# Optimization experiments

Hardware: AMD Instinct MI355X
Metric: run time of the kernel (lower is better)

The kernel has to match this reference:

```python
import jax, jax.numpy as jnp
import numpy as np

N_HEAD = 12


def setup_inputs() -> dict:
    key = jax.random.key(0)
    ks = jax.random.split(key, 5)
    B, T, C = 2, 2048, 768
    x = jax.random.normal(ks[0], (B, T, C), dtype=jnp.float32)
    w_attn = jax.random.normal(ks[1], (3 * C, C), dtype=jnp.float32) * 0.02
    b_attn = jax.random.normal(ks[2], (3 * C,), dtype=jnp.float32) * 0.02
    w_proj = jax.random.normal(ks[3], (C, C), dtype=jnp.float32) * 0.02
    b_proj = jax.random.normal(ks[4], (C,), dtype=jnp.float32) * 0.02
    return {"x": x, "w_attn": w_attn, "b_attn": b_attn, "w_proj": w_proj, "b_proj": b_proj}


def reference(x, w_attn, b_attn, w_proj, b_proj):
    B, T, C = x.shape
    H = N_HEAD
    D = C // H
    # fused QKV projection (torch Linear: x @ W.T + b)
    qkv = x @ w_attn.T + b_attn                      # [B, T, 3C]
    q, k, v = jnp.split(qkv, 3, axis=-1)
    q = q.reshape(B, T, H, D).transpose(0, 2, 1, 3)  # [B, H, T, D]
    k = k.reshape(B, T, H, D).transpose(0, 2, 1, 3)
    v = v.reshape(B, T, H, D).transpose(0, 2, 1, 3)
    # NOTE: original scales by 1/sqrt(k.size(0)) == 1/sqrt(B) (batch!), reproduced faithfully
    scale = 1.0 / jnp.sqrt(jnp.asarray(B, dtype=x.dtype))
    scores = jnp.einsum("bhtd,bhsd->bhts", q, k) * scale  # [B, H, T, T]
    causal = jnp.tril(jnp.ones((T, T), dtype=bool))
    scores = jnp.where(causal[None, None], scores, jnp.asarray(-jnp.inf, dtype=x.dtype))
    attn = jax.nn.softmax(scores, axis=-1)
    # dropout layers are identity in eval mode
    out = jnp.einsum("bhts,bhsd->bhtd", attn, v)     # [B, H, T, D]
    out = out.transpose(0, 2, 1, 3).reshape(B, T, C)
    return out @ w_proj.T + b_proj
```

## Files before the change

kernel.cpp:

```cpp
#include <hip/hip_runtime.h>
#include <hip/hip_bf16.h>
#include <stdint.h>

typedef __bf16 bf16;
typedef __bf16 bf16x4 __attribute__((ext_vector_type(4)));
typedef __bf16 bf16x8 __attribute__((ext_vector_type(8)));
typedef float f32x4 __attribute__((ext_vector_type(4)));

__device__ __forceinline__ f32x4 mfma16(bf16x8 a, bf16x8 b, f32x4 c) {
    return __builtin_amdgcn_mfma_f32_16x16x32_bf16(a, b, c, 0, 0, 0);
}

__device__ __forceinline__ void gload_lds16(const void* g, void* l) {
    __builtin_amdgcn_global_load_lds((__attribute__((address_space(1))) void*)g,
                                     (__attribute__((address_space(3))) void*)l,
                                     16, 0, 0);
}

__global__ void k_cast3(const float* __restrict__ x, const float* __restrict__ wa,
                        const float* __restrict__ wp, bf16* __restrict__ xb,
                        bf16* __restrict__ wab, bf16* __restrict__ wpb) {
    const int N1 = 786432, N2 = 442368, N3 = 147456;
    int i = blockIdx.x * blockDim.x + threadIdx.x;
    int stride = gridDim.x * blockDim.x;
    for (; i < N1 + N2 + N3; i += stride) {
        const float* src; bf16* dst; int j = i;
        if (j < N1)           { src = x;  dst = xb; }
        else if (j < N1 + N2) { src = wa; dst = wab; j -= N1; }
        else                  { src = wp; dst = wpb; j -= N1 + N2; }
        float4 v = reinterpret_cast<const float4*>(src)[j];
        bf16x4 o = { (bf16)v.x, (bf16)v.y, (bf16)v.z, (bf16)v.w };
        reinterpret_cast<bf16x4*>(dst)[j] = o;
    }
}

template<bool BF16_OUT>
__global__ __launch_bounds__(256) void k_gemm_bt(
        const bf16* __restrict__ A, const bf16* __restrict__ W,
        const float* __restrict__ bias, void* __restrict__ Cout,
        int M, int N, int K) {
    __shared__ bf16 As[128 * 32];
    __shared__ bf16 Ws[128 * 32];
    const int tid = threadIdx.x;
    const int l = tid & 63, w = tid >> 6;
    const int lr = l & 15, lq = l >> 4;
    const int wm = w >> 1, wn = w & 1;
    const int bm = blockIdx.y * 128, bn = blockIdx.x * 128;

    f32x4 acc[4][4] = {};

    for (int k0 = 0; k0 < K; k0 += 32) {
        __syncthreads();
        #pragma unroll
        for (int i = 0; i < 2; ++i) {
            int c = tid + i * 256;
            int row = c >> 2, c8 = (c & 3) * 8;
            gload_lds16(A + (size_t)(bm + row) * K + k0 + c8, As + c * 8);
            gload_lds16(W + (size_t)(bn + row) * K + k0 + c8, Ws + c * 8);
        }
        __syncthreads();
        bf16x8 af[4], wf[4];
        #pragma unroll
        for (int f = 0; f < 4; ++f) {
            af[f] = *reinterpret_cast<const bf16x8*>(As + (wm * 64 + f * 16 + lr) * 32 + lq * 8);
            wf[f] = *reinterpret_cast<const bf16x8*>(Ws + (wn * 64 + f * 16 + lr) * 32 + lq * 8);
        }
        #pragma unroll
        for (int fm = 0; fm < 4; ++fm)
            #pragma unroll
            for (int fn = 0; fn < 4; ++fn)
                acc[fm][fn] = mfma16(af[fm], wf[fn], acc[fm][fn]);
    }

    #pragma unroll
    for (int fm = 0; fm < 4; ++fm) {
        #pragma unroll
        for (int fn = 0; fn < 4; ++fn) {
            int row = bm + wm * 64 + fm * 16 + lq * 4;
            int col = bn + wn * 64 + fn * 16 + lr;
            float bv = bias[col];
            #pragma unroll
            for (int r = 0; r < 4; ++r) {
                float v = acc[fm][fn][r] + bv;
                if (BF16_OUT)
                    ((bf16*)Cout)[(size_t)(row + r) * N + col] = (bf16)v;
                else
                    ((float*)Cout)[(size_t)(row + r) * N + col] = v;
            }
        }
    }
}

#define CLOG2E 1.02014439f

__global__ __launch_bounds__(256, 3) void k_flash_attn(
        const bf16* __restrict__ qkv, bf16* __restrict__ att) {
    __shared__ bf16 Ks[3][4096];
    __shared__ bf16 Vt[2][64][72];

    const int tid = threadIdx.x;
    const int l = tid & 63, w = tid >> 6;
    const int lr = l & 15, lq = l >> 4;

    const int bid = blockIdx.x;
    const int s = bid >> 8, i = (bid >> 3) & 31, t7 = bid & 7;
    int qb;
    if (s == 0)      qb = i;
    else if (s == 2) qb = (i + 16) & 31;
    else             qb = (i < 8) ? (31 - 2 * i) : (i < 16) ? (30 - 2 * i)
                       : (i < 24) ? (62 - 2 * i) : (63 - 2 * i);
    const int hb = s * 8 + t7;
    const int h = hb % 12, b = hb / 12;

    const bf16* Qp = qkv + (size_t)b * 2048 * 2304 + h * 64;
    const bf16* Kp = Qp + 768;
    const bf16* Vp = Qp + 1536;

    const int qr0 = qb * 64 + w * 16;

    bf16x8 qf[2];
    #pragma unroll
    for (int ks = 0; ks < 2; ++ks)
        qf[ks] = *reinterpret_cast<const bf16x8*>(
            Qp + (size_t)(qr0 + lr) * 2304 + ks * 32 + lq * 8);

    f32x4 o[4] = {};
    float lsum = 0.f;

    auto stageK = [&](int buf, int kv0) {
        #pragma unroll
        for (int ii = 0; ii < 2; ++ii) {
            int c = tid + ii * 256;
            int row = c >> 3, j = c & 7;
            gload_lds16(Kp + (size_t)(kv0 + row) * 2304 + ((j ^ (row & 7)) * 8),
                        &Ks[buf][c * 8]);
        }
    };
    bf16x8 vv0, vv1;
    auto loadV = [&](int kv0) {
        vv0 = *reinterpret_cast<const bf16x8*>(
            Vp + (size_t)(kv0 + (tid >> 3)) * 2304 + (tid & 7) * 8);
        vv1 = *reinterpret_cast<const bf16x8*>(
            Vp + (size_t)(kv0 + 32 + (tid >> 3)) * 2304 + (tid & 7) * 8);
    };
    auto writeV = [&](int buf) {
        int kv = tid >> 3, d0 = (tid & 7) * 8;
        int sw = (tid & 7) << 3;
        #pragma unroll
        for (int j = 0; j < 8; ++j) {
            int d = d0 + j;
            Vt[buf][d][kv ^ sw]        = vv0[j];
            Vt[buf][d][(kv + 32) ^ sw] = vv1[j];
        }
    };

    const int ntiles = qb + 1;

    stageK(0, 0);
    if (ntiles > 1) stageK(1, 64);
    loadV(0);
    asm volatile("s_waitcnt vmcnt(0)" ::: "memory");
    writeV(0);
    asm volatile("s_waitcnt lgkmcnt(0)" ::: "memory");
    __builtin_amdgcn_s_barrier();
    asm volatile("" ::: "memory");

    for (int jt = 0; jt < ntiles; ++jt) {
        const int curV = jt & 1;
        const int curK = jt % 3;
        const int kv0 = jt * 64;
        if (jt + 1 < ntiles) loadV(kv0 + 64);
        if (jt + 2 < ntiles) stageK((jt + 2) % 3, kv0 + 128);

        const bool diag = (jt == qb);
        const int rsw = lr & 7;
        float p[4][4];
        __builtin_amdgcn_s_setprio(1);
        #pragma unroll
        for (int t = 0; t < 4; ++t) {
            f32x4 sacc = {0.f, 0.f, 0.f, 0.f};
            #pragma unroll
            for (int ks = 0; ks < 2; ++ks) {
                bf16x8 kf = *reinterpret_cast<const bf16x8*>(
                    &Ks[curK][(t * 16 + lr) * 64 + (((ks * 4 + lq) ^ rsw) * 8)]);
                sacc = mfma16(kf, qf[ks], sacc);
            }
            #pragma unroll
            for (int r = 0; r < 4; ++r) {
                float e = exp2f(sacc[r] * CLOG2E);
                if (diag && (t * 16 + lq * 4 + r > w * 16 + lr)) e = 0.f;
                p[t][r] = e;
                lsum += e;
            }
        }
        __builtin_amdgcn_s_setprio(0);

        unsigned P0[4], P1[4];
        #pragma unroll
        for (int t = 0; t < 4; ++t) {
            asm("v_cvt_pk_bf16_f32 %0, %1, %2" : "=v"(P0[t]) : "v"(p[t][0]), "v"(p[t][1]));
            asm("v_cvt_pk_bf16_f32 %0, %1, %2" : "=v"(P1[t]) : "v"(p[t][2]), "v"(p[t][3]));
        }
        __builtin_amdgcn_s_setprio(1);
        #pragma unroll
        for (int ks = 0; ks < 2; ++ks) {
            unsigned a0 = P0[2 * ks], b0 = P0[2 * ks + 1];
            asm volatile("v_permlane32_swap_b32 %0, %1" : "+v"(a0), "+v"(b0));
            asm volatile("v_permlane16_swap_b32 %0, %1" : "+v"(a0), "+v"(b0));
            unsigned a1 = P1[2 * ks], b1 = P1[2 * ks + 1];
            asm volatile("v_permlane32_swap_b32 %0, %1" : "+v"(a1), "+v"(b1));
            asm volatile("v_permlane16_swap_b32 %0, %1" : "+v"(a1), "+v"(b1));
            union { unsigned u[4]; bf16x8 v8; } pk_;
            pk_.u[0] = a0; pk_.u[1] = a1; pk_.u[2] = b0; pk_.u[3] = b1;
            bf16x8 pa = pk_.v8;
            #pragma unroll
            for (int db = 0; db < 4; ++db) {
                int row = db * 16 + lr;
                bf16x8 vf = *reinterpret_cast<const bf16x8*>(
                    &Vt[curV][row][(ks * 32 + lq * 8) ^ (((row >> 3) & 7) << 3)]);
                o[db] = mfma16(pa, vf, o[db]);
            }
        }
        __builtin_amdgcn_s_setprio(0);

        if (jt + 1 < ntiles) writeV(curV ^ 1);
        asm volatile("s_waitcnt lgkmcnt(0)" ::: "memory");
        __builtin_amdgcn_s_barrier();
        asm volatile("" ::: "memory");
    }

    lsum += __shfl_xor(lsum, 16);
    lsum += __shfl_xor(lsum, 32);
    float inv[4];
    #pragma unroll
    for (int r = 0; r < 4; ++r)
        inv[r] = 1.0f / __shfl(lsum, lq * 4 + r);

    #pragma unroll
    for (int db = 0; db < 4; ++db)
        #pragma unroll
        for (int r = 0; r < 4; ++r) {
            float v = o[db][r] * inv[r];
            att[(size_t)(b * 2048 + qr0 + lq * 4 + r) * 768 + h * 64 + db * 16 + lr] = (bf16)v;
        }
}

extern "C" void kernel_launch(void* const* d_in, const int* in_sizes, int n_in,
                              void* d_out, int out_size, void* d_ws, size_t ws_size,
                              hipStream_t stream) {
    const float* x      = (const float*)d_in[0];
    const float* w_attn = (const float*)d_in[1];
    const float* b_attn = (const float*)d_in[2];
    const float* w_proj = (const float*)d_in[3];
    const float* b_proj = (const float*)d_in[4];

    char* ws = (char*)d_ws;
    bf16* xb  = (bf16*)(ws + 0);
    bf16* wab = (bf16*)(ws + 6291456);
    bf16* wpb = (bf16*)(ws + 9830400);
    bf16* qkv = (bf16*)(ws + 11010048);
    bf16* att = (bf16*)(ws + 29884416);

    k_cast3<<<2048, 256, 0, stream>>>(x, w_attn, w_proj, xb, wab, wpb);

    dim3 g1(2304 / 128, 4096 / 128);
    k_gemm_bt<true><<<g1, 256, 0, stream>>>(xb, wab, b_attn, qkv, 4096, 2304, 768);

    k_flash_attn<<<768, 256, 0, stream>>>(qkv, att);

    dim3 g2(768 / 128, 4096 / 128);
    k_gemm_bt<false><<<g2, 256, 0, stream>>>(att, wpb, b_proj, d_out, 4096, 768, 768);
}
```

Before: 105.7 us.

## Split long causal attention rows across two blocks and deepen GEMM K-tile with swizzle

Attention query blocks 16-31 are split into two KV-range halves that write unnormalized partial outputs and row sums to a workspace, and a new reduce kernel combines them. This is meant to balance per-block work across the causal triangle and raise the block count. The GEMM K-step grows from 32 to 64 with an XOR-swizzled LDS layout to halve barrier count and avoid bank conflicts, and exp2f becomes the hardware builtin. The split costs an extra launch plus fp32 partial traffic, and it only runs when the workspace is large enough.

```diff
diff --git a/kernel.cpp b/kernel.cpp
--- a/kernel.cpp
+++ b/kernel.cpp
@@ -39,8 +39,8 @@
         const bf16* __restrict__ A, const bf16* __restrict__ W,
         const float* __restrict__ bias, void* __restrict__ Cout,
         int M, int N, int K) {
-    __shared__ bf16 As[128 * 32];
-    __shared__ bf16 Ws[128 * 32];
+    __shared__ bf16 As[128 * 64];
+    __shared__ bf16 Ws[128 * 64];
     const int tid = threadIdx.x;
     const int l = tid & 63, w = tid >> 6;
     const int lr = l & 15, lq = l >> 4;
@@ -49,27 +49,36 @@
 
     f32x4 acc[4][4] = {};
 
-    for (int k0 = 0; k0 < K; k0 += 32) {
+    for (int k0 = 0; k0 < K; k0 += 64) {
         __syncthreads();
         #pragma unroll
-        for (int i = 0; i < 2; ++i) {
+        for (int i = 0; i < 4; ++i) {
             int c = tid + i * 256;
-            int row = c >> 2, c8 = (c & 3) * 8;
-            gload_lds16(A + (size_t)(bm + row) * K + k0 + c8, As + c * 8);
-            gload_lds16(W + (size_t)(bn + row) * K + k0 + c8, Ws + c * 8);
+            int row = c >> 3, j = c & 7;
+            int src8 = (j ^ (row & 7)) * 8;
+            gload_lds16(A + (size_t)(bm + row) * K + k0 + src8, As + c * 8);
+            gload_lds16(W + (size_t)(bn + row) * K + k0 + src8, Ws + c * 8);
         }
         __syncthreads();
-        bf16x8 af[4], wf[4];
-        #pragma unroll
-        for (int f = 0; f < 4; ++f) {
-            af[f] = *reinterpret_cast<const bf16x8*>(As + (wm * 64 + f * 16 + lr) * 32 + lq * 8);
-            wf[f] = *reinterpret_cast<const bf16x8*>(Ws + (wn * 64 + f * 16 + lr) * 32 + lq * 8);
-        }
-        #pragma unroll
-        for (int fm = 0; fm < 4; ++fm)
-            #pragma unroll
-            for (int fn = 0; fn < 4; ++fn)
-                acc[fm][fn] = mfma16(af[fm], wf[fn], acc[fm][fn]);
+        bf16x8 af[2][4], wf[2][4];
+        #pragma unroll
+        for (int ks = 0; ks < 2; ++ks)
+            #pragma unroll
+            for (int f = 0; f < 4; ++f) {
+                int ra = wm * 64 + f * 16 + lr;
+                int rb = wn * 64 + f * 16 + lr;
+                af[ks][f] = *reinterpret_cast<const bf16x8*>(
+                    As + ra * 64 + (((ks * 4 + lq) ^ (lr & 7)) * 8));
+                wf[ks][f] = *reinterpret_cast<const bf16x8*>(
+                    Ws + rb * 64 + (((ks * 4 + lq) ^ (lr & 7)) * 8));
+            }
+        #pragma unroll
+        for (int ks = 0; ks < 2; ++ks)
+            #pragma unroll
+            for (int fm = 0; fm < 4; ++fm)
+                #pragma unroll
+                for (int fn = 0; fn < 4; ++fn)
+                    acc[fm][fn] = mfma16(af[ks][fm], wf[ks][fn], acc[fm][fn]);
     }
 
     #pragma unroll
@@ -94,7 +103,8 @@
 #define CLOG2E 1.02014439f
 
 __global__ __launch_bounds__(256, 3) void k_flash_attn(
-        const bf16* __restrict__ qkv, bf16* __restrict__ att) {
+        const bf16* __restrict__ qkv, bf16* __restrict__ att,
+        float* __restrict__ part, int mode) {
     __shared__ bf16 Ks[3][4096];
     __shared__ bf16 Vt[2][64][72];
 
@@ -103,14 +113,24 @@
     const int lr = l & 15, lq = l >> 4;
 
     const int bid = blockIdx.x;
-    const int s = bid >> 8, i = (bid >> 3) & 31, t7 = bid & 7;
-    int qb;
-    if (s == 0)      qb = i;
-    else if (s == 2) qb = (i + 16) & 31;
-    else             qb = (i < 8) ? (31 - 2 * i) : (i < 16) ? (30 - 2 * i)
-                       : (i < 24) ? (62 - 2 * i) : (63 - 2 * i);
-    const int hb = s * 8 + t7;
-    const int h = hb % 12, b = hb / 12;
+    int qb, h, b, jt0, jt1, slot;
+    bool dopart;
+    if (mode) {
+        int bh = bid % 24, idx = bid / 24;
+        h = bh % 12; b = bh / 12;
+        if (idx < 16)      { qb = 16 + idx;  jt0 = 0;  jt1 = 16;     dopart = true;  slot = (bh * 16 + idx) * 2; }
+        else if (idx < 32) { qb = 47 - idx;  jt0 = 16; jt1 = qb + 1; dopart = true;  slot = (bh * 16 + (qb - 16)) * 2 + 1; }
+        else               { qb = 47 - idx;  jt0 = 0;  jt1 = qb + 1; dopart = false; slot = 0; }
+    } else {
+        const int s = bid >> 8, i = (bid >> 3) & 31, t7 = bid & 7;
+        if (s == 0)      qb = i;
+        else if (s == 2) qb = (i + 16) & 31;
+        else             qb = (i < 8) ? (31 - 2 * i) : (i < 16) ? (30 - 2 * i)
+                           : (i < 24) ? (62 - 2 * i) : (63 - 2 * i);
+        const int hb = s * 8 + t7;
+        h = hb % 12; b = hb / 12;
+        jt0 = 0; jt1 = qb + 1; dopart = false; slot = 0;
+    }
 
     const bf16* Qp = qkv + (size_t)b * 2048 * 2304 + h * 64;
     const bf16* Kp = Qp + 768;
@@ -154,23 +174,21 @@
         }
     };
 
-    const int ntiles = qb + 1;
-
-    stageK(0, 0);
-    if (ntiles > 1) stageK(1, 64);
-    loadV(0);
+    stageK(0, jt0 * 64);
+    if (jt1 > jt0 + 1) stageK(1, (jt0 + 1) * 64);
+    loadV(jt0 * 64);
     asm volatile("s_waitcnt vmcnt(0)" ::: "memory");
     writeV(0);
     asm volatile("s_waitcnt lgkmcnt(0)" ::: "memory");
     __builtin_amdgcn_s_barrier();
     asm volatile("" ::: "memory");
 
-    for (int jt = 0; jt < ntiles; ++jt) {
-        const int curV = jt & 1;
-        const int curK = jt % 3;
+    for (int jt = jt0; jt < jt1; ++jt) {
+        const int curV = (jt - jt0) & 1;
+        const int curK = (jt - jt0) % 3;
         const int kv0 = jt * 64;
-        if (jt + 1 < ntiles) loadV(kv0 + 64);
-        if (jt + 2 < ntiles) stageK((jt + 2) % 3, kv0 + 128);
+        if (jt + 1 < jt1) loadV(kv0 + 64);
+        if (jt + 2 < jt1) stageK((jt + 2 - jt0) % 3, kv0 + 128);
 
         const bool diag = (jt == qb);
         const int rsw = lr & 7;
@@ -187,7 +205,7 @@
             }
             #pragma unroll
             for (int r = 0; r < 4; ++r) {
-                float e = exp2f(sacc[r] * CLOG2E);
+                float e = __builtin_amdgcn_exp2f(sacc[r] * CLOG2E);
                 if (diag && (t * 16 + lq * 4 + r > w * 16 + lr)) e = 0.f;
                 p[t][r] = e;
                 lsum += e;
@@ -223,7 +241,7 @@
         }
         __builtin_amdgcn_s_setprio(0);
 
-        if (jt + 1 < ntiles) writeV(curV ^ 1);
+        if (jt + 1 < jt1) writeV(curV ^ 1);
         asm volatile("s_waitcnt lgkmcnt(0)" ::: "memory");
         __builtin_amdgcn_s_barrier();
         asm volatile("" ::: "memory");
@@ -231,18 +249,43 @@
 
     lsum += __shfl_xor(lsum, 16);
     lsum += __shfl_xor(lsum, 32);
-    float inv[4];
-    #pragma unroll
-    for (int r = 0; r < 4; ++r)
-        inv[r] = 1.0f / __shfl(lsum, lq * 4 + r);
-
-    #pragma unroll
-    for (int db = 0; db < 4; ++db)
-        #pragma unroll
-        for (int r = 0; r < 4; ++r) {
-            float v = o[db][r] * inv[r];
-            att[(size_t)(b * 2048 + qr0 + lq * 4 + r) * 768 + h * 64 + db * 16 + lr] = (bf16)v;
-        }
+
+    if (dopart) {
+        float* pb = part + (size_t)slot * 4160;
+        #pragma unroll
+        for (int db = 0; db < 4; ++db)
+            #pragma unroll
+            for (int r = 0; r < 4; ++r)
+                pb[(w * 16 + lq * 4 + r) * 64 + db * 16 + lr] = o[db][r];
+        if (lq == 0) pb[4096 + w * 16 + lr] = lsum;
+    } else {
+        float inv[4];
+        #pragma unroll
+        for (int r = 0; r < 4; ++r)
+            inv[r] = 1.0f / __shfl(lsum, lq * 4 + r);
+        #pragma unroll
+        for (int db = 0; db < 4; ++db)
+            #pragma unroll
+            for (int r = 0; r < 4; ++r) {
+                float v = o[db][r] * inv[r];
+                att[(size_t)(b * 2048 + qr0 + lq * 4 + r) * 768 + h * 64 + db * 16 + lr] = (bf16)v;
+            }
+    }
+}
+
+__global__ __launch_bounds__(256) void k_attn_reduce(
+        const float* __restrict__ part, bf16* __restrict__ att) {
+    int g = blockIdx.x;
+    int bh = g / 16, q16 = g % 16, qb = 16 + q16;
+    int h = bh % 12, b = bh / 12;
+    const float* p0 = part + (size_t)((bh * 16 + q16) * 2) * 4160;
+    const float* p1 = p0 + 4160;
+    for (int e = threadIdx.x; e < 4096; e += 256) {
+        int row = e >> 6, col = e & 63;
+        float O = p0[e] + p1[e];
+        float L = p0[4096 + row] + p1[4096 + row];
+        att[(size_t)(b * 2048 + qb * 64 + row) * 768 + h * 64 + col] = (bf16)(O / L);
+    }
 }
 
 extern "C" void kernel_launch(void* const* d_in, const int* in_sizes, int n_in,
@@ -255,18 +298,25 @@
     const float* b_proj = (const float*)d_in[4];
 
     char* ws = (char*)d_ws;
-    bf16* xb  = (bf16*)(ws + 0);
-    bf16* wab = (bf16*)(ws + 6291456);
-    bf16* wpb = (bf16*)(ws + 9830400);
-    bf16* qkv = (bf16*)(ws + 11010048);
-    bf16* att = (bf16*)(ws + 29884416);
+    bf16* xb   = (bf16*)(ws + 0);
+    bf16* wab  = (bf16*)(ws + 6291456);
+    bf16* wpb  = (bf16*)(ws + 9830400);
+    bf16* qkv  = (bf16*)(ws + 11010048);
+    bf16* att  = (bf16*)(ws + 29884416);
+    float* part = (float*)(ws + 36175872);
+    const unsigned long long WS_NEEDED = 36175872ull + 12779520ull;
 
     k_cast3<<<2048, 256, 0, stream>>>(x, w_attn, w_proj, xb, wab, wpb);
 
     dim3 g1(2304 / 128, 4096 / 128);
     k_gemm_bt<true><<<g1, 256, 0, stream>>>(xb, wab, b_attn, qkv, 4096, 2304, 768);
 
-    k_flash_attn<<<768, 256, 0, stream>>>(qkv, att);
+    if (ws_size >= WS_NEEDED) {
+        k_flash_attn<<<1152, 256, 0, stream>>>(qkv, att, part, 1);
+        k_attn_reduce<<<384, 256, 0, stream>>>(part, att);
+    } else {
+        k_flash_attn<<<768, 256, 0, stream>>>(qkv, att, part, 0);
+    }
 
     dim3 g2(768 / 128, 4096 / 128);
     k_gemm_bt<false><<<g2, 256, 0, stream>>>(att, wpb, b_proj, d_out, 4096, 768, 768);
```

New measurement: 88.39 us. 1.2x faster.
